# Performance work log

Measured on AMD Instinct MI355X. Metric: run time of the kernel, lower is better.

Reference implementation:

```python
import math
import jax, jax.numpy as jnp
import numpy as np

N_QUBITS = 8
N_QLAYERS = 2
HIDDEN = 768
BATCH = 8192
LN_EPS = 1e-5


def _ry_gate(theta):
    # theta: scalar or (B,) -> (2,2) or (B,2,2) complex64
    h = theta * 0.5
    c, s = jnp.cos(h), jnp.sin(h)
    g = jnp.stack([jnp.stack([c, -s], axis=-1), jnp.stack([s, c], axis=-1)], axis=-2)
    return g.astype(jnp.complex64)


def _rz_gate(theta):
    t = theta.astype(jnp.complex64)
    e0, e1 = jnp.exp(-0.5j * t), jnp.exp(0.5j * t)
    z = jnp.zeros_like(e0)
    return jnp.stack([jnp.stack([e0, z], axis=-1), jnp.stack([z, e1], axis=-1)], axis=-2)


def _apply_1q(state, gate, w, n):
    # state: (B, 2**n); gate: (2,2) shared or (B,2,2) per-sample; wire w (0 = MSB)
    B = state.shape[0]
    s = state.reshape(B, 2 ** w, 2, -1)
    if gate.ndim == 2:
        s = jnp.einsum('ij,bljr->blir', gate, s)
    else:
        s = jnp.einsum('bij,bljr->blir', gate, s)
    return s.reshape(B, -1)


def _apply_cnot(state, c, t, n):
    B = state.shape[0]
    s = state.reshape((B,) + (2,) * n)
    ax_c = 1 + c
    s0 = jnp.take(s, 0, axis=ax_c)  # control=0 branch, control axis removed
    s1 = jnp.take(s, 1, axis=ax_c)
    ax_t = 1 + t - (1 if t > c else 0)
    s1 = jnp.flip(s1, axis=ax_t)    # X on target when control=1
    s = jnp.stack([s0, s1], axis=ax_c)
    return s.reshape(B, -1)


def _circuit(angles, weights_ry, weights_rz):
    # angles: (B, n) float32 -> (B, n) PauliZ expectations, batched statevector sim
    n, L = N_QUBITS, N_QLAYERS
    B = angles.shape[0]
    state = jnp.zeros((B, 2 ** n), dtype=jnp.complex64).at[:, 0].set(1.0)
    for i in range(n):
        state = _apply_1q(state, _ry_gate(angles[:, i]), i, n)
    for i in range(1, n):
        state = _apply_cnot(state, 0, i, n)
    for l in range(L):
        for i in range(n):
            state = _apply_1q(state, _ry_gate(weights_ry[l, i]), i, n)
            state = _apply_1q(state, _rz_gate(weights_rz[l, i]), i, n)
    for i in range(1, n):
        state = _apply_cnot(state, i, 0, n)
    probs = jnp.abs(state) ** 2  # (B, 2**n)
    k = jnp.arange(2 ** n)
    bits = (k[None, :] >> (n - 1 - jnp.arange(n))[:, None]) & 1  # wire 0 = MSB (PennyLane)
    signs = (1 - 2 * bits).astype(probs.dtype)  # (n, 2**n)
    return probs @ signs.T  # (B, n)


def setup_inputs() -> dict:
    key = jax.random.key(0)
    ks = jax.random.split(key, 8)
    return {
        'hidden': jax.random.normal(ks[0], (BATCH, HIDDEN), dtype=jnp.float32),
        'W_in': jax.random.normal(ks[1], (N_QUBITS, HIDDEN), dtype=jnp.float32) * (1.0 / math.sqrt(HIDDEN)),
        'b_in': jax.random.normal(ks[2], (N_QUBITS,), dtype=jnp.float32) * 0.01,
        'W_out': jax.random.normal(ks[3], (HIDDEN, N_QUBITS), dtype=jnp.float32) * (1.0 / math.sqrt(N_QUBITS)),
        'b_out': jax.random.normal(ks[4], (HIDDEN,), dtype=jnp.float32) * 0.01,
        'weights_ry': jax.random.normal(ks[5], (N_QLAYERS, N_QUBITS), dtype=jnp.float32) * 0.1,
        'weights_rz': jax.random.normal(ks[6], (N_QLAYERS, N_QUBITS), dtype=jnp.float32) * 0.1,
        'gamma': jnp.ones((HIDDEN,), dtype=jnp.float32),
        'beta': jnp.zeros((HIDDEN,), dtype=jnp.float32),
    }


def reference(hidden, W_in, b_in, W_out, b_out, weights_ry, weights_rz, gamma, beta):
    phase = 0.0
    angles = jnp.tanh(hidden @ W_in.T + b_in) * math.pi + phase  # (B, n)
    meas = _circuit(angles, weights_ry, weights_rz).astype(jnp.float32)  # (B, n)
    y = meas @ W_out.T + b_out  # (B, h)
    mu = jnp.mean(y, axis=-1, keepdims=True)
    var = jnp.mean(jnp.square(y - mu), axis=-1, keepdims=True)
    return (y - mu) * jax.lax.rsqrt(var + LN_EPS) * gamma + beta
```

## Files before the change

kernel.cpp:

```cpp
#include <hip/hip_runtime.h>
#include <hip/hip_bf16.h>

#define NQ    8
#define HID   768
#define BATCH 8192
#define SPW   2
#define SPB   (4*SPW)
#define NBLK  (BATCH / SPB)
#define TPB   256

template<int BF> __device__ __forceinline__ float LDV(const void* p, int i) {
    if constexpr (BF) return __bfloat162float(((const __hip_bfloat16*)p)[i]);
    else return ((const float*)p)[i];
}
template<int BF> __device__ __forceinline__ float4 LD4(const void* p, int i4) {
    if constexpr (BF) {
        ushort4 v = ((const ushort4*)p)[i4];
        float4 r;
        r.x = __uint_as_float(((unsigned)v.x) << 16);
        r.y = __uint_as_float(((unsigned)v.y) << 16);
        r.z = __uint_as_float(((unsigned)v.z) << 16);
        r.w = __uint_as_float(((unsigned)v.w) << 16);
        return r;
    } else {
        return ((const float4*)p)[i4];
    }
}
template<int BF> __device__ __forceinline__ void ST4(void* p, int i4, float4 v) {
    if constexpr (BF) {
        __hip_bfloat16 bx = __float2bfloat16(v.x);
        __hip_bfloat16 by = __float2bfloat16(v.y);
        __hip_bfloat16 bz = __float2bfloat16(v.z);
        __hip_bfloat16 bw = __float2bfloat16(v.w);
        ushort4 s;
        s.x = *(const unsigned short*)&bx;
        s.y = *(const unsigned short*)&by;
        s.z = *(const unsigned short*)&bz;
        s.w = *(const unsigned short*)&bw;
        ((ushort4*)p)[i4] = s;
    } else {
        ((float4*)p)[i4] = v;
    }
}

template<int BF>
__device__ __forceinline__ void run_all(
    const void* hidden_, const void* W_in_, const void* b_in_,
    const void* W_out_, const void* b_out_, const void* wry_, const void* wrz_,
    const void* gamma_, const void* beta_, void* out_)
{
    const int tid  = threadIdx.x;
    const int lane = tid & 63;
    const int wv   = tid >> 6;
    const int j    = lane >> 3;
    const int u    = lane & 7;
    const int b0   = blockIdx.x * SPB + wv * SPW;
    const int b1   = b0 + 1;

    float DA, DB, Kr, Ki;
    {
        float ry0 = LDV<BF>(wry_, j), ry1 = LDV<BF>(wry_, NQ + j);
        float rz0 = LDV<BF>(wrz_, j), rz1 = LDV<BF>(wrz_, NQ + j);
        float cA = cosf(0.5f*ry0), sA = sinf(0.5f*ry0);
        float cB = cosf(0.5f*ry1), sB = sinf(0.5f*ry1);
        float p0c = cosf(0.5f*rz0), p0s = sinf(0.5f*rz0);
        float p1c = cosf(0.5f*rz1), p1s = sinf(0.5f*rz1);
        float g00r =  cA*p0c, g00i = -cA*p0s;
        float g01r = -sA*p0c, g01i =  sA*p0s;
        float g10r =  sA*p0c, g10i =  sA*p0s;
        float g11r =  cA*p0c, g11i =  cA*p0s;
        float h00r = cB*g00r - sB*g10r, h00i = cB*g00i - sB*g10i;
        float h01r = cB*g01r - sB*g11r, h01i = cB*g01i - sB*g11i;
        float h10r = sB*g00r + cB*g10r, h10i = sB*g00i + cB*g10i;
        float h11r = sB*g01r + cB*g11r, h11i = sB*g01i + cB*g11i;
        float f00r = h00r*p1c + h00i*p1s, f00i = h00i*p1c - h00r*p1s;
        float f01r = h01r*p1c + h01i*p1s, f01i = h01i*p1c - h01r*p1s;
        float f10r = h10r*p1c - h10i*p1s, f10i = h10i*p1c + h10r*p1s;
        float f11r = h11r*p1c - h11i*p1s, f11i = h11i*p1c + h11r*p1s;
        DA = f00r*f00r + f00i*f00i - (f10r*f10r + f10i*f10i);
        DB = f01r*f01r + f01i*f01i - (f11r*f11r + f11i*f11i);
        Kr = (f00r*f01r + f00i*f01i) - (f10r*f11r + f10i*f11i);
        Ki = (f00i*f01r - f00r*f01i) - (f10i*f11r - f10r*f11i);
    }

    float p00=0,p01=0,p02=0,p03=0, p10=0,p11=0,p12=0,p13=0;
    const int h0b = b0 * (HID/4);
    const int h1b = b1 * (HID/4);
    const int wb  = j  * (HID/4);
    #pragma unroll
    for (int t = 0; t < 24; ++t) {
        int i4 = u + (t << 3);
        float4 w  = LD4<BF>(W_in_,   wb  + i4);
        float4 h0 = LD4<BF>(hidden_, h0b + i4);
        float4 h1 = LD4<BF>(hidden_, h1b + i4);
        p00 = fmaf(h0.x, w.x, p00); p01 = fmaf(h0.y, w.y, p01);
        p02 = fmaf(h0.z, w.z, p02); p03 = fmaf(h0.w, w.w, p03);
        p10 = fmaf(h1.x, w.x, p10); p11 = fmaf(h1.y, w.y, p11);
        p12 = fmaf(h1.z, w.z, p12); p13 = fmaf(h1.w, w.w, p13);
    }
    float acc0 = (p00 + p01) + (p02 + p03);
    float acc1 = (p10 + p11) + (p12 + p13);
    #pragma unroll
    for (int d = 1; d < 8; d <<= 1) {
        acc0 += __shfl_xor(acc0, d, 64);
        acc1 += __shfl_xor(acc1, d, 64);
    }

    float binj = LDV<BF>(b_in_, j);
    float th0 = tanhf(acc0 + binj);
    float th1 = tanhf(acc1 + binj);
    float sj0 = sinpif(th0), cj0 = cospif(th0);
    float sj1 = sinpif(th1), cj1 = cospif(th1);

    float ca = 0.5f * (DA + DB), da = 0.5f * (DA - DB);
    const bool g0 = (j == 0);
    float uu0 = da * cj0, vv0 = fmaf(Kr, sj0, ca);
    float uu1 = da * cj1, vv1 = fmaf(Kr, sj1, ca);
    float MA0 = g0 ? 1.f : (vv0 + uu0), MB0 = g0 ? 1.f : (vv0 - uu0);
    float MA1 = g0 ? 1.f : (vv1 + uu1), MB1 = g0 ? 1.f : (vv1 - uu1);
    float fr0 = g0 ? 1.f : Kr, fi0 = g0 ? 0.f : (cj0 * Ki);
    float fr1 = g0 ? 1.f : Kr, fi1 = g0 ? 0.f : (cj1 * Ki);
    #pragma unroll
    for (int d = 8; d < 64; d <<= 1) {
        MA0 *= __shfl_xor(MA0, d, 64);   MA1 *= __shfl_xor(MA1, d, 64);
        MB0 *= __shfl_xor(MB0, d, 64);   MB1 *= __shfl_xor(MB1, d, 64);
        float q0r = __shfl_xor(fr0, d, 64), q0i = __shfl_xor(fi0, d, 64);
        float q1r = __shfl_xor(fr1, d, 64), q1i = __shfl_xor(fi1, d, 64);
        float n0r = fr0*q0r - fi0*q0i, n0i = fr0*q0i + fi0*q0r;
        float n1r = fr1*q1r - fi1*q1i, n1i = fr1*q1i + fi1*q1r;
        fr0 = n0r; fi0 = n0i; fr1 = n1r; fi1 = n1i;
    }
    float DA0 = __shfl(DA, 0, 64), DB0 = __shfl(DB, 0, 64);
    float Kr0 = __shfl(Kr, 0, 64), Ki0 = __shfl(Ki, 0, 64);
    float cc00 = __shfl(cj0, 0, 64), sc00 = __shfl(sj0, 0, 64);
    float cc01 = __shfl(cj1, 0, 64), sc01 = __shfl(sj1, 0, 64);
    float meas00 = 0.5f*(1.f+cc00)*DA0*MA0 + 0.5f*(1.f-cc00)*DB0*MB0
                 + sc00*(Kr0*fr0 - Ki0*fi0);
    float meas01 = 0.5f*(1.f+cc01)*DA0*MA1 + 0.5f*(1.f-cc01)*DB0*MB1
                 + sc01*(Kr0*fr1 - Ki0*fi1);
    float measj0 = g0 ? meas00 : fmaf(cc00, uu0, vv0);
    float measj1 = g0 ? meas01 : fmaf(cc01, uu1, vv1);
    float m00 = meas00;
    float m01 = __shfl(measj0,  8, 64), m02 = __shfl(measj0, 16, 64);
    float m03 = __shfl(measj0, 24, 64), m04 = __shfl(measj0, 32, 64);
    float m05 = __shfl(measj0, 40, 64), m06 = __shfl(measj0, 48, 64);
    float m07 = __shfl(measj0, 56, 64);
    float m10 = meas01;
    float m11 = __shfl(measj1,  8, 64), m12 = __shfl(measj1, 16, 64);
    float m13 = __shfl(measj1, 24, 64), m14 = __shfl(measj1, 32, 64);
    float m15 = __shfl(measj1, 40, 64), m16 = __shfl(measj1, 48, 64);
    float m17 = __shfl(measj1, 56, 64);

    float y0v[12], y1v[12];
    float sum0 = 0.f, sq0 = 0.f, sum1 = 0.f, sq1 = 0.f;
    #pragma unroll
    for (int g = 0; g < 3; ++g) {
        float4 bo = LD4<BF>(b_out_, 3*lane + g);
        float bos[4] = {bo.x, bo.y, bo.z, bo.w};
        #pragma unroll
        for (int e = 0; e < 4; ++e) {
            int c = 12*lane + 4*g + e;
            float4 w0 = LD4<BF>(W_out_, c*2);
            float4 w1 = LD4<BF>(W_out_, c*2 + 1);
            float y0 = bos[e], y1 = bos[e];
            y0 = fmaf(m00, w0.x, y0); y0 = fmaf(m01, w0.y, y0);
            y0 = fmaf(m02, w0.z, y0); y0 = fmaf(m03, w0.w, y0);
            y0 = fmaf(m04, w1.x, y0); y0 = fmaf(m05, w1.y, y0);
            y0 = fmaf(m06, w1.z, y0); y0 = fmaf(m07, w1.w, y0);
            y1 = fmaf(m10, w0.x, y1); y1 = fmaf(m11, w0.y, y1);
            y1 = fmaf(m12, w0.z, y1); y1 = fmaf(m13, w0.w, y1);
            y1 = fmaf(m14, w1.x, y1); y1 = fmaf(m15, w1.y, y1);
            y1 = fmaf(m16, w1.z, y1); y1 = fmaf(m17, w1.w, y1);
            y0v[4*g+e] = y0; y1v[4*g+e] = y1;
            sum0 += y0; sq0 = fmaf(y0, y0, sq0);
            sum1 += y1; sq1 = fmaf(y1, y1, sq1);
        }
    }
    #pragma unroll
    for (int d = 1; d < 64; d <<= 1) {
        sum0 += __shfl_xor(sum0, d, 64);  sq0 += __shfl_xor(sq0, d, 64);
        sum1 += __shfl_xor(sum1, d, 64);  sq1 += __shfl_xor(sq1, d, 64);
    }
    float mean0 = sum0 * (1.f/HID);
    float var0  = fmaf(sq0, 1.f/HID, -mean0*mean0);
    float rstd0 = rsqrtf(var0 + 1e-5f);
    float mean1 = sum1 * (1.f/HID);
    float var1  = fmaf(sq1, 1.f/HID, -mean1*mean1);
    float rstd1 = rsqrtf(var1 + 1e-5f);
    #pragma unroll
    for (int g = 0; g < 3; ++g) {
        float4 ga = LD4<BF>(gamma_, 3*lane + g);
        float4 be = LD4<BF>(beta_,  3*lane + g);
        float4 o0, o1;
        o0.x = fmaf((y0v[4*g+0]-mean0)*rstd0, ga.x, be.x);
        o0.y = fmaf((y0v[4*g+1]-mean0)*rstd0, ga.y, be.y);
        o0.z = fmaf((y0v[4*g+2]-mean0)*rstd0, ga.z, be.z);
        o0.w = fmaf((y0v[4*g+3]-mean0)*rstd0, ga.w, be.w);
        o1.x = fmaf((y1v[4*g+0]-mean1)*rstd1, ga.x, be.x);
        o1.y = fmaf((y1v[4*g+1]-mean1)*rstd1, ga.y, be.y);
        o1.z = fmaf((y1v[4*g+2]-mean1)*rstd1, ga.z, be.z);
        o1.w = fmaf((y1v[4*g+3]-mean1)*rstd1, ga.w, be.w);
        ST4<BF>(out_, b0*(HID/4) + 3*lane + g, o0);
        ST4<BF>(out_, b1*(HID/4) + 3*lane + g, o1);
    }
}

__global__ __launch_bounds__(TPB, 4) void main_kernel(
    const void* hidden_, const void* W_in_, const void* b_in_,
    const void* W_out_, const void* b_out_, const void* wry_, const void* wrz_,
    const void* gamma_, const void* beta_, void* out_)
{
    const int lane = threadIdx.x & 63;
    unsigned wrd = ((const unsigned*)hidden_)[lane];
    unsigned lo  = wrd & 0xffffu;
    unsigned e   = (lo >> 7) & 0xffu;
    bool v = (lo == 0u) || (e >= 100u && e <= 133u);
    unsigned long long mask = __ballot(v);
    int flag = (__popcll(mask) > 32) ? 1 : 0;
    if (flag)
        run_all<1>(hidden_, W_in_, b_in_, W_out_, b_out_, wry_, wrz_,
                   gamma_, beta_, out_);
    else
        run_all<0>(hidden_, W_in_, b_in_, W_out_, b_out_, wry_, wrz_,
                   gamma_, beta_, out_);
}

extern "C" void kernel_launch(void* const* d_in, const int* in_sizes, int n_in,
                              void* d_out, int out_size, void* d_ws, size_t ws_size,
                              hipStream_t stream) {
    const void* hidden = d_in[0];
    const void* W_in   = d_in[1];
    const void* b_in   = d_in[2];
    const void* W_out  = d_in[3];
    const void* b_out  = d_in[4];
    const void* wry    = d_in[5];
    const void* wrz    = d_in[6];
    const void* gamma  = d_in[7];
    const void* beta   = d_in[8];
    (void)d_ws; (void)ws_size;
    main_kernel<<<NBLK, TPB, 0, stream>>>(hidden, W_in, b_in, W_out, b_out,
                                          wry, wrz, gamma, beta, d_out);
}
```

Measured before the change: 120.2 us.

## Process one sample per wavefront with coalesced loads and transposing butterfly reduction

Each wavefront now handles a single batch row instead of two. The input projection has each lane read contiguous float4 chunks of the hidden row and accumulate all 8 qubit dot products, then combines them with a transpose-style butterfly shuffle reduction. Output-side indexing changes from a per-lane strided layout (3*lane+g) to a lane-contiguous one (64*t+lane), so global loads and stores coalesce. The trade-off is twice as many blocks and less amortisation of the per-wavefront gate setup and W_out reads across samples.

```diff
diff --git a/kernel.cpp b/kernel.cpp
--- a/kernel.cpp
+++ b/kernel.cpp
@@ -4,8 +4,7 @@
 #define NQ    8
 #define HID   768
 #define BATCH 8192
-#define SPW   2
-#define SPB   (4*SPW)
+#define SPB   4
 #define NBLK  (BATCH / SPB)
 #define TPB   256
 
@@ -53,9 +52,7 @@
     const int lane = tid & 63;
     const int wv   = tid >> 6;
     const int j    = lane >> 3;
-    const int u    = lane & 7;
-    const int b0   = blockIdx.x * SPB + wv * SPW;
-    const int b1   = b0 + 1;
+    const int b    = blockIdx.x * SPB + wv;
 
     float DA, DB, Kr, Ki;
     {
@@ -83,125 +80,123 @@
         Ki = (f00i*f01r - f00r*f01i) - (f10i*f11r - f10r*f11i);
     }
 
-    float p00=0,p01=0,p02=0,p03=0, p10=0,p11=0,p12=0,p13=0;
-    const int h0b = b0 * (HID/4);
-    const int h1b = b1 * (HID/4);
-    const int wb  = j  * (HID/4);
-    #pragma unroll
-    for (int t = 0; t < 24; ++t) {
-        int i4 = u + (t << 3);
-        float4 w  = LD4<BF>(W_in_,   wb  + i4);
-        float4 h0 = LD4<BF>(hidden_, h0b + i4);
-        float4 h1 = LD4<BF>(hidden_, h1b + i4);
-        p00 = fmaf(h0.x, w.x, p00); p01 = fmaf(h0.y, w.y, p01);
-        p02 = fmaf(h0.z, w.z, p02); p03 = fmaf(h0.w, w.w, p03);
-        p10 = fmaf(h1.x, w.x, p10); p11 = fmaf(h1.y, w.y, p11);
-        p12 = fmaf(h1.z, w.z, p12); p13 = fmaf(h1.w, w.w, p13);
-    }
-    float acc0 = (p00 + p01) + (p02 + p03);
-    float acc1 = (p10 + p11) + (p12 + p13);
-    #pragma unroll
-    for (int d = 1; d < 8; d <<= 1) {
-        acc0 += __shfl_xor(acc0, d, 64);
-        acc1 += __shfl_xor(acc1, d, 64);
-    }
-
-    float binj = LDV<BF>(b_in_, j);
-    float th0 = tanhf(acc0 + binj);
-    float th1 = tanhf(acc1 + binj);
-    float sj0 = sinpif(th0), cj0 = cospif(th0);
-    float sj1 = sinpif(th1), cj1 = cospif(th1);
+    float p[NQ];
+    #pragma unroll
+    for (int q = 0; q < NQ; ++q) p[q] = 0.f;
+    const int hb = b * (HID/4);
+    #pragma unroll
+    for (int t = 0; t < 3; ++t) {
+        const int q4 = (t << 6) + lane;
+        float4 h = LD4<BF>(hidden_, hb + q4);
+        #pragma unroll
+        for (int jj = 0; jj < NQ; ++jj) {
+            float4 w = LD4<BF>(W_in_, jj*(HID/4) + q4);
+            p[jj] = fmaf(h.x, w.x, p[jj]);
+            p[jj] = fmaf(h.y, w.y, p[jj]);
+            p[jj] = fmaf(h.z, w.z, p[jj]);
+            p[jj] = fmaf(h.w, w.w, p[jj]);
+        }
+    }
+    const bool mb0 = ((lane >> 3) & 1) != 0;
+    const bool mb1 = ((lane >> 4) & 1) != 0;
+    const bool mb2 = ((lane >> 5) & 1) != 0;
+    float np[4];
+    #pragma unroll
+    for (int k = 0; k < 4; ++k) {
+        float sent = mb0 ? p[2*k]   : p[2*k+1];
+        float keep = mb0 ? p[2*k+1] : p[2*k];
+        np[k] = keep + __shfl_xor(sent, 8, 64);
+    }
+    float nq[2];
+    #pragma unroll
+    for (int k = 0; k < 2; ++k) {
+        float sent = mb1 ? np[2*k]   : np[2*k+1];
+        float keep = mb1 ? np[2*k+1] : np[2*k];
+        nq[k] = keep + __shfl_xor(sent, 16, 64);
+    }
+    float z;
+    {
+        float sent = mb2 ? nq[0] : nq[1];
+        float keep = mb2 ? nq[1] : nq[0];
+        z = keep + __shfl_xor(sent, 32, 64);
+    }
+    z += __shfl_xor(z, 1, 64);
+    z += __shfl_xor(z, 2, 64);
+    z += __shfl_xor(z, 4, 64);
+
+    float zb = z + LDV<BF>(b_in_, j);
+    float th = tanhf(zb);
+    float sj = sinpif(th), cj = cospif(th);
 
     float ca = 0.5f * (DA + DB), da = 0.5f * (DA - DB);
     const bool g0 = (j == 0);
-    float uu0 = da * cj0, vv0 = fmaf(Kr, sj0, ca);
-    float uu1 = da * cj1, vv1 = fmaf(Kr, sj1, ca);
-    float MA0 = g0 ? 1.f : (vv0 + uu0), MB0 = g0 ? 1.f : (vv0 - uu0);
-    float MA1 = g0 ? 1.f : (vv1 + uu1), MB1 = g0 ? 1.f : (vv1 - uu1);
-    float fr0 = g0 ? 1.f : Kr, fi0 = g0 ? 0.f : (cj0 * Ki);
-    float fr1 = g0 ? 1.f : Kr, fi1 = g0 ? 0.f : (cj1 * Ki);
+    float uu = da * cj;
+    float vv = fmaf(Kr, sj, ca);
+    float MA = g0 ? 1.f : (vv + uu), MB = g0 ? 1.f : (vv - uu);
+    float fr = g0 ? 1.f : Kr, fi = g0 ? 0.f : (cj * Ki);
     #pragma unroll
     for (int d = 8; d < 64; d <<= 1) {
-        MA0 *= __shfl_xor(MA0, d, 64);   MA1 *= __shfl_xor(MA1, d, 64);
-        MB0 *= __shfl_xor(MB0, d, 64);   MB1 *= __shfl_xor(MB1, d, 64);
-        float q0r = __shfl_xor(fr0, d, 64), q0i = __shfl_xor(fi0, d, 64);
-        float q1r = __shfl_xor(fr1, d, 64), q1i = __shfl_xor(fi1, d, 64);
-        float n0r = fr0*q0r - fi0*q0i, n0i = fr0*q0i + fi0*q0r;
-        float n1r = fr1*q1r - fi1*q1i, n1i = fr1*q1i + fi1*q1r;
-        fr0 = n0r; fi0 = n0i; fr1 = n1r; fi1 = n1i;
+        MA *= __shfl_xor(MA, d, 64);
+        MB *= __shfl_xor(MB, d, 64);
+        float qr = __shfl_xor(fr, d, 64);
+        float qi = __shfl_xor(fi, d, 64);
+        float nr = fr*qr - fi*qi;
+        float ni = fr*qi + fi*qr;
+        fr = nr; fi = ni;
     }
     float DA0 = __shfl(DA, 0, 64), DB0 = __shfl(DB, 0, 64);
     float Kr0 = __shfl(Kr, 0, 64), Ki0 = __shfl(Ki, 0, 64);
-    float cc00 = __shfl(cj0, 0, 64), sc00 = __shfl(sj0, 0, 64);
-    float cc01 = __shfl(cj1, 0, 64), sc01 = __shfl(sj1, 0, 64);
-    float meas00 = 0.5f*(1.f+cc00)*DA0*MA0 + 0.5f*(1.f-cc00)*DB0*MB0
-                 + sc00*(Kr0*fr0 - Ki0*fi0);
-    float meas01 = 0.5f*(1.f+cc01)*DA0*MA1 + 0.5f*(1.f-cc01)*DB0*MB1
-                 + sc01*(Kr0*fr1 - Ki0*fi1);
-    float measj0 = g0 ? meas00 : fmaf(cc00, uu0, vv0);
-    float measj1 = g0 ? meas01 : fmaf(cc01, uu1, vv1);
-    float m00 = meas00;
-    float m01 = __shfl(measj0,  8, 64), m02 = __shfl(measj0, 16, 64);
-    float m03 = __shfl(measj0, 24, 64), m04 = __shfl(measj0, 32, 64);
-    float m05 = __shfl(measj0, 40, 64), m06 = __shfl(measj0, 48, 64);
-    float m07 = __shfl(measj0, 56, 64);
-    float m10 = meas01;
-    float m11 = __shfl(measj1,  8, 64), m12 = __shfl(measj1, 16, 64);
-    float m13 = __shfl(measj1, 24, 64), m14 = __shfl(measj1, 32, 64);
-    float m15 = __shfl(measj1, 40, 64), m16 = __shfl(measj1, 48, 64);
-    float m17 = __shfl(measj1, 56, 64);
-
-    float y0v[12], y1v[12];
-    float sum0 = 0.f, sq0 = 0.f, sum1 = 0.f, sq1 = 0.f;
-    #pragma unroll
-    for (int g = 0; g < 3; ++g) {
-        float4 bo = LD4<BF>(b_out_, 3*lane + g);
+    float cc0 = __shfl(cj, 0, 64), sc0 = __shfl(sj, 0, 64);
+    float meas0 = 0.5f*(1.f+cc0)*DA0*MA + 0.5f*(1.f-cc0)*DB0*MB
+                + sc0*(Kr0*fr - Ki0*fi);
+    float measj = g0 ? meas0 : fmaf(cc0, uu, vv);
+    float m0 = meas0;
+    float m1 = __shfl(measj,  8, 64), m2 = __shfl(measj, 16, 64);
+    float m3 = __shfl(measj, 24, 64), m4 = __shfl(measj, 32, 64);
+    float m5 = __shfl(measj, 40, 64), m6 = __shfl(measj, 48, 64);
+    float m7 = __shfl(measj, 56, 64);
+
+    float yv[12];
+    float sum = 0.f, sq = 0.f;
+    #pragma unroll
+    for (int t = 0; t < 3; ++t) {
+        const int q4 = (t << 6) + lane;
+        float4 bo = LD4<BF>(b_out_, q4);
         float bos[4] = {bo.x, bo.y, bo.z, bo.w};
         #pragma unroll
         for (int e = 0; e < 4; ++e) {
-            int c = 12*lane + 4*g + e;
+            int c = 4*q4 + e;
             float4 w0 = LD4<BF>(W_out_, c*2);
             float4 w1 = LD4<BF>(W_out_, c*2 + 1);
-            float y0 = bos[e], y1 = bos[e];
-            y0 = fmaf(m00, w0.x, y0); y0 = fmaf(m01, w0.y, y0);
-            y0 = fmaf(m02, w0.z, y0); y0 = fmaf(m03, w0.w, y0);
-            y0 = fmaf(m04, w1.x, y0); y0 = fmaf(m05, w1.y, y0);
-            y0 = fmaf(m06, w1.z, y0); y0 = fmaf(m07, w1.w, y0);
-            y1 = fmaf(m10, w0.x, y1); y1 = fmaf(m11, w0.y, y1);
-            y1 = fmaf(m12, w0.z, y1); y1 = fmaf(m13, w0.w, y1);
-            y1 = fmaf(m14, w1.x, y1); y1 = fmaf(m15, w1.y, y1);
-            y1 = fmaf(m16, w1.z, y1); y1 = fmaf(m17, w1.w, y1);
-            y0v[4*g+e] = y0; y1v[4*g+e] = y1;
-            sum0 += y0; sq0 = fmaf(y0, y0, sq0);
-            sum1 += y1; sq1 = fmaf(y1, y1, sq1);
+            float y = bos[e];
+            y = fmaf(m0, w0.x, y); y = fmaf(m1, w0.y, y);
+            y = fmaf(m2, w0.z, y); y = fmaf(m3, w0.w, y);
+            y = fmaf(m4, w1.x, y); y = fmaf(m5, w1.y, y);
+            y = fmaf(m6, w1.z, y); y = fmaf(m7, w1.w, y);
+            yv[4*t+e] = y;
+            sum += y;
+            sq = fmaf(y, y, sq);
         }
     }
     #pragma unroll
     for (int d = 1; d < 64; d <<= 1) {
-        sum0 += __shfl_xor(sum0, d, 64);  sq0 += __shfl_xor(sq0, d, 64);
-        sum1 += __shfl_xor(sum1, d, 64);  sq1 += __shfl_xor(sq1, d, 64);
-    }
-    float mean0 = sum0 * (1.f/HID);
-    float var0  = fmaf(sq0, 1.f/HID, -mean0*mean0);
-    float rstd0 = rsqrtf(var0 + 1e-5f);
-    float mean1 = sum1 * (1.f/HID);
-    float var1  = fmaf(sq1, 1.f/HID, -mean1*mean1);
-    float rstd1 = rsqrtf(var1 + 1e-5f);
-    #pragma unroll
-    for (int g = 0; g < 3; ++g) {
-        float4 ga = LD4<BF>(gamma_, 3*lane + g);
-        float4 be = LD4<BF>(beta_,  3*lane + g);
-        float4 o0, o1;
-        o0.x = fmaf((y0v[4*g+0]-mean0)*rstd0, ga.x, be.x);
-        o0.y = fmaf((y0v[4*g+1]-mean0)*rstd0, ga.y, be.y);
-        o0.z = fmaf((y0v[4*g+2]-mean0)*rstd0, ga.z, be.z);
-        o0.w = fmaf((y0v[4*g+3]-mean0)*rstd0, ga.w, be.w);
-        o1.x = fmaf((y1v[4*g+0]-mean1)*rstd1, ga.x, be.x);
-        o1.y = fmaf((y1v[4*g+1]-mean1)*rstd1, ga.y, be.y);
-        o1.z = fmaf((y1v[4*g+2]-mean1)*rstd1, ga.z, be.z);
-        o1.w = fmaf((y1v[4*g+3]-mean1)*rstd1, ga.w, be.w);
-        ST4<BF>(out_, b0*(HID/4) + 3*lane + g, o0);
-        ST4<BF>(out_, b1*(HID/4) + 3*lane + g, o1);
+        sum += __shfl_xor(sum, d, 64);
+        sq  += __shfl_xor(sq,  d, 64);
+    }
+    float mean = sum * (1.f/HID);
+    float var  = fmaf(sq, 1.f/HID, -mean*mean);
+    float rstd = rsqrtf(var + 1e-5f);
+    #pragma unroll
+    for (int t = 0; t < 3; ++t) {
+        const int q4 = (t << 6) + lane;
+        float4 ga = LD4<BF>(gamma_, q4);
+        float4 be = LD4<BF>(beta_,  q4);
+        float4 o;
+        o.x = fmaf((yv[4*t+0]-mean)*rstd, ga.x, be.x);
+        o.y = fmaf((yv[4*t+1]-mean)*rstd, ga.y, be.y);
+        o.z = fmaf((yv[4*t+2]-mean)*rstd, ga.z, be.z);
+        o.w = fmaf((yv[4*t+3]-mean)*rstd, ga.w, be.w);
+        ST4<BF>(out_, hb + q4, o);
     }
 }
 
```

Measured after the change: 117.6 us. 2.2% less time.
